# Optimization experiments

Hardware: AMD Instinct MI355X
Metric: run time of the kernel (lower is better)

Reference implementation:

```python
import jax, jax.numpy as jnp
import numpy as np

N_NODE = 4096   # nodes per graph (generalized from hardcoded 55)
IN_DIM = 200    # input_dim, forced by attn1 in_channel=200
OUT_DIM = 200   # output_dim, forced equal to input_dim by GRU_gate shapes
N_HEADS = 8     # forced by attn2 in_channel 1600 = 8*200
SEQ_LEN = 4
HID = 200       # hid_units default


def _glorot(k, shape):
    r = np.sqrt(6.0 / (shape[0] + shape[1])).astype(np.float32)
    return jax.random.uniform(k, shape, jnp.float32, -r, r)


def setup_inputs() -> dict:
    key = jax.random.key(0)
    ks = jax.random.split(key, 32)
    inp = {}
    mask = jax.random.bernoulli(ks[0], 0.01, (SEQ_LEN, N_NODE, N_NODE))
    inp['adjs'] = jax.random.uniform(ks[1], (SEQ_LEN, N_NODE, N_NODE), jnp.float32) * mask
    inp['feats'] = jax.random.normal(ks[2], (SEQ_LEN, N_NODE, IN_DIM), jnp.float32)
    inp['p_covss'] = jnp.zeros((SEQ_LEN,), jnp.float32)  # passed but unused in original
    # per-head weight_vars, randn(output_dim, input_dim) in original call()
    inp['init_wv'] = jax.random.normal(ks[3], (N_HEADS, OUT_DIM, IN_DIM), jnp.float32)
    # attn1 (shared across all heads): conv1d(k=1) == linear
    inp['W1'] = _glorot(ks[4], (HID, IN_DIM)); inp['b1'] = jnp.zeros((HID,), jnp.float32)
    inp['a11'] = _glorot(ks[5], (HID, 1))[:, 0]; inp['a11b'] = jnp.zeros((), jnp.float32)
    inp['a12'] = _glorot(ks[6], (HID, 1))[:, 0]; inp['a12b'] = jnp.zeros((), jnp.float32)
    # attn2
    inp['W2'] = _glorot(ks[7], (OUT_DIM, N_HEADS * HID)); inp['b2'] = jnp.zeros((OUT_DIM,), jnp.float32)
    inp['a21'] = _glorot(ks[8], (OUT_DIM, 1))[:, 0]; inp['a21b'] = jnp.zeros((), jnp.float32)
    inp['a22'] = _glorot(ks[9], (OUT_DIM, 1))[:, 0]; inp['a22b'] = jnp.zeros((), jnp.float32)
    # GRU gates (reset/update/htilda), reduce=True since n_node != input_dim
    for i, g in enumerate(['r', 'u', 'h']):
        inp['W' + g] = _glorot(ks[10 + 4 * i], (N_NODE, OUT_DIM))
        inp['U' + g] = _glorot(ks[11 + 4 * i], (OUT_DIM, OUT_DIM))
        inp['P' + g] = _glorot(ks[12 + 4 * i], (IN_DIM, N_NODE))
        inp['b' + g] = jnp.zeros((IN_DIM, OUT_DIM), jnp.float32)
    return inp


def reference(adjs, feats, p_covss, init_wv, W1, b1, a11, a11b, a12, a12b,
              W2, b2, a21, a21b, a22, a22b,
              Wr, Ur, Pr, br, Wu, Uu, Pu, bu, Wh, Uh, Ph, bh):
    def gat(x):  # x: [N, IN_DIM]
        fts = x @ W1.T + b1                                   # [N, HID]
        # logits f_1 + f_2^T on [N,1,1] stays [N,1,1]; softmax over the
        # singleton dim is identically 1 -> attention is degenerate.
        s = jax.nn.leaky_relu((fts @ a11 + a11b) + (fts @ a12 + a12b), 0.01)
        coefs = jnp.ones_like(s)                              # softmax([N,1,1], dim=1)
        h = jax.nn.elu(coefs[:, None] * fts)                  # [N, HID]
        hcat = jnp.tile(h, (1, N_HEADS))                      # heads share attn1 -> identical
        fts2 = hcat @ W2.T + b2                               # [N, OUT_DIM]
        s2 = jax.nn.leaky_relu((fts2 @ a21 + a21b) + (fts2 @ a22 + a22b), 0.01)
        coefs2 = jnp.ones_like(s2)
        out = jax.nn.elu(coefs2[:, None] * fts2)              # [N, OUT_DIM]
        # torch: out.view(nb_classes, -1).T then softmax(dim=1), then view(-1, out_dim)
        logits = jnp.reshape(out, (OUT_DIM, N_NODE)).T        # memory reinterpretation, not transpose
        return jax.nn.softmax(logits, axis=1)                 # [N, OUT_DIM]

    embeds = jax.vmap(gat)(feats)                             # [T, N, OUT_DIM]

    def gru_step(wv, adj):  # wv: [H, OUT_DIM, IN_DIM=OUT_DIM], adj: [N, N]
        # head-independent sparse propagation bases, one per gate
        gr = Pr @ (adj @ Wr) + br                             # [IN_DIM, OUT_DIM]
        gu = Pu @ (adj @ Wu) + bu
        gh = Ph @ (adj @ Wh) + bh
        r = jax.nn.sigmoid(gr + wv @ Ur)                      # [H, 200, 200]
        u = jax.nn.sigmoid(gu + wv @ Uu)
        hcap = jnp.tanh(gh + (r * wv) @ Uh)
        return (1.0 - u) * wv + u * hcap, None

    final_wv, _ = jax.lax.scan(gru_step, init_wv, adjs[1:])   # evolve over t=1..T-1
    return embeds, final_wv
```

## Files before the change

### kernel.cpp

```cpp
#include <hip/hip_runtime.h>
#include <hip/hip_bf16.h>
#include <math.h>

typedef __hip_bfloat16 bf16;
typedef __attribute__((ext_vector_type(8))) short short8;
typedef __attribute__((ext_vector_type(4))) float f32x4;

#define N_NODE 4096
#define DIM 200
#define NH 8
#define SEQ 4
#define TLDA 40

__device__ __forceinline__ float eluf(float x) { return x > 0.f ? x : expm1f(x); }
__device__ __forceinline__ float sigm(float x) { return 1.f / (1.f + expf(-x)); }

template<bool ISB>
__device__ __forceinline__ float ldv(const void* p, size_t i) {
    if (ISB) return __bfloat162float(((const bf16*)p)[i]);
    else     return ((const float*)p)[i];
}
template<bool ISB>
__device__ __forceinline__ void stv(void* p, size_t i, float v) {
    if (ISB) ((bf16*)p)[i] = __float2bfloat16(v);
    else     ((float*)p)[i] = v;
}
__device__ __forceinline__ float bflo(unsigned u) { return __uint_as_float((u & 0xffffu) << 16); }
__device__ __forceinline__ float bfhi(unsigned u) { return __uint_as_float(u & 0xffff0000u); }
__device__ __forceinline__ short f2bs(float v) {
    bf16 h = __float2bfloat16(v);
    return *(short*)&h;
}

__global__ void k_detect(const void* feats, int* flag) {
    __shared__ int cnt;
    if (threadIdx.x == 0) cnt = 0;
    __syncthreads();
    const unsigned short* u = (const unsigned short*)feats;
    unsigned short v = u[2 * threadIdx.x];
    int e = (v >> 7) & 0xFF;
    if (e >= 100 && e <= 140) atomicAdd(&cnt, 1);
    __syncthreads();
    if (threadIdx.x == 0) *flag = (cnt >= 128) ? 1 : 0;
}


template<int AMODE>
__device__ __forceinline__ short8 ldA8x(const void* A, int lda, int arow, bool rowOK,
                                        int kk, int K) {
    short8 r;
    if (rowOK && kk + 8 <= K) {
        if (AMODE == 1) {
            r = *(const short8*)((const short*)A + (size_t)arow * lda + kk);
        } else {
            const float* ap = (const float*)A + (size_t)arow * lda + kk;
            float4 f0 = *(const float4*)ap;
            float4 f1 = *(const float4*)(ap + 4);
            r[0] = f2bs(f0.x); r[1] = f2bs(f0.y); r[2] = f2bs(f0.z); r[3] = f2bs(f0.w);
            r[4] = f2bs(f1.x); r[5] = f2bs(f1.y); r[6] = f2bs(f1.z); r[7] = f2bs(f1.w);
        }
    } else {
#pragma unroll
        for (int j = 0; j < 8; j++) {
            bool ok = rowOK && kk + j < K;
            if (AMODE == 1) r[j] = ok ? ((const short*)A)[(size_t)arow * lda + kk + j] : (short)0;
            else            r[j] = ok ? f2bs(((const float*)A)[(size_t)arow * lda + kk + j]) : (short)0;
        }
    }
    return r;
}

template<int BMODE>
__device__ __forceinline__ short8 ldB8x(const void* B, int gcol, bool colOK,
                                        int kk, int K) {
    short8 r;
    if (BMODE == 2) {
        if (colOK && kk + 8 <= K) {
            r = *(const short8*)((const short*)B + (size_t)gcol * K + kk);
        } else {
#pragma unroll
            for (int j = 0; j < 8; j++)
                r[j] = (colOK && kk + j < K) ? ((const short*)B)[(size_t)gcol * K + kk + j] : (short)0;
        }
    } else {
#pragma unroll
        for (int j = 0; j < 8; j++)
            r[j] = (colOK && kk + j < K) ? ((const short*)B)[(size_t)(kk + j) * DIM + gcol] : (short)0;
    }
    return r;
}

__device__ __forceinline__ short8 ldUfrag(const short* U, int col, int k) {
    if (k + 8 <= 200) return *(const short8*)(U + col * 200 + k);
    short8 z = {};
    return z;
}

template<int EPI, int AMODE, int BMODE, int CB16>
__device__ void mgemm(short* As, short* Bs,
                      const void* A, int lda, const void* B, int M, int K,
                      int kbeg, int kend, const float* X1,
                      void* Cv, int row0, int c0) {
    const int N = DIM;
    int tid = threadIdx.x;
    int wave = tid >> 6, lane = tid & 63;
    int m16 = lane & 15, q = lane >> 4;
    int s_row = tid >> 2;
    int s_k   = (tid & 3) * 8;
    int b_col = tid & 63;
    int b_kg  = (tid >> 6) * 8;
    int arow = row0 + s_row;
    bool rowOK = arow < M;
    int gcol = c0 + b_col;
    bool colOK = gcol < N;
    short8 la = ldA8x<AMODE>(A, lda, arow, rowOK, kbeg + s_k, K);
    short8 lb = ldB8x<BMODE>(B, gcol, colOK, kbeg + b_kg, K);
    f32x4 acc[4] = {};
    for (int k0 = kbeg; k0 < kend; k0 += 32) {
        __syncthreads();
        *(short8*)&As[s_row * TLDA + s_k] = la;
        *(short8*)&Bs[b_col * TLDA + b_kg] = lb;
        __syncthreads();
        int kn = k0 + 32;
        if (kn < kend) {
            la = ldA8x<AMODE>(A, lda, arow, rowOK, kn + s_k, K);
            lb = ldB8x<BMODE>(B, gcol, colOK, kn + b_kg, K);
        }
        short8 bfr = *(short8*)&Bs[(wave * 16 + m16) * TLDA + q * 8];
#pragma unroll
        for (int r = 0; r < 4; r++) {
            short8 af = *(short8*)&As[(r * 16 + m16) * TLDA + q * 8];
            acc[r] = __builtin_amdgcn_mfma_f32_16x16x32_bf16(af, bfr, acc[r], 0, 0, 0);
        }
    }
    int colw = c0 + wave * 16 + m16;
    if (colw >= N) return;
#pragma unroll
    for (int r = 0; r < 4; r++) {
        int rowb = row0 + r * 16 + q * 4;
#pragma unroll
        for (int reg = 0; reg < 4; reg++) {
            int row = rowb + reg;
            if (row >= M) continue;
            float v = acc[r][reg];
            size_t ci = (size_t)row * 200 + colw;
            if (EPI == 0) {
                float o = eluf(v + X1[colw]);
                if (CB16) ((short*)Cv)[ci] = f2bs(o);
                else      ((float*)Cv)[ci] = o;
            } else {
                atomicAdd(&((float*)Cv)[ci], v);
            }
        }
    }
}

template<bool ISB>
__device__ void aw_body(char* smemc, const void* adjs, const unsigned short* Wcat,
                        bf16* AWb, int i, int s) {
    size_t arow = ((size_t)(s + 1) * N_NODE + i) * N_NODE;
    int*   s_k   = (int*)smemc;
    float* s_v   = (float*)(smemc + 2048);
    int*   s_cnt = (int*)(smemc + 4096);
    int tid = threadIdx.x;
    if (tid == 0) *s_cnt = 0;
    __syncthreads();
    float vals[16];
#pragma unroll
    for (int c = 0; c < 4; c++) {
        int col = c * 1024 + tid * 4;
        if (ISB) {
            ushort4 u = *(const ushort4*)((const unsigned short*)adjs + arow + col);
            vals[c*4+0] = __uint_as_float((unsigned)u.x << 16);
            vals[c*4+1] = __uint_as_float((unsigned)u.y << 16);
            vals[c*4+2] = __uint_as_float((unsigned)u.z << 16);
            vals[c*4+3] = __uint_as_float((unsigned)u.w << 16);
        } else {
            float4 f = *(const float4*)((const float*)adjs + arow + col);
            vals[c*4+0] = f.x; vals[c*4+1] = f.y; vals[c*4+2] = f.z; vals[c*4+3] = f.w;
        }
    }
#pragma unroll
    for (int q = 0; q < 16; q++) {
        if (vals[q] != 0.f) {
            int p = atomicAdd(s_cnt, 1);
            if (p < 512) { s_k[p] = (q >> 2) * 1024 + tid * 4 + (q & 3); s_v[p] = vals[q]; }
        }
    }
    __syncthreads();
    int n = *s_cnt < 512 ? *s_cnt : 512;
    float a0 = 0.f, a1 = 0.f, d0 = 0.f, d1 = 0.f;
    bool hasB = (tid < 44);
    int offA = 2 * tid, offB = 512 + 2 * tid;
    int e = 0;
    for (; e + 4 <= n; e += 4) {
        int   k0 = s_k[e],   k1 = s_k[e+1], k2 = s_k[e+2], k3 = s_k[e+3];
        float v0 = s_v[e],   v1 = s_v[e+1], v2 = s_v[e+2], v3 = s_v[e+3];
        unsigned wa0 = *(const unsigned*)(Wcat + (size_t)k0 * 608 + offA);
        unsigned wa1 = *(const unsigned*)(Wcat + (size_t)k1 * 608 + offA);
        unsigned wa2 = *(const unsigned*)(Wcat + (size_t)k2 * 608 + offA);
        unsigned wa3 = *(const unsigned*)(Wcat + (size_t)k3 * 608 + offA);
        if (hasB) {
            unsigned wb0 = *(const unsigned*)(Wcat + (size_t)k0 * 608 + offB);
            unsigned wb1 = *(const unsigned*)(Wcat + (size_t)k1 * 608 + offB);
            unsigned wb2 = *(const unsigned*)(Wcat + (size_t)k2 * 608 + offB);
            unsigned wb3 = *(const unsigned*)(Wcat + (size_t)k3 * 608 + offB);
            d0 += v0*bflo(wb0) + v1*bflo(wb1) + v2*bflo(wb2) + v3*bflo(wb3);
            d1 += v0*bfhi(wb0) + v1*bfhi(wb1) + v2*bfhi(wb2) + v3*bfhi(wb3);
        }
        a0 += v0*bflo(wa0) + v1*bflo(wa1) + v2*bflo(wa2) + v3*bflo(wa3);
        a1 += v0*bfhi(wa0) + v1*bfhi(wa1) + v2*bfhi(wa2) + v3*bfhi(wa3);
    }
    for (; e < n; e++) {
        int k = s_k[e]; float v = s_v[e];
        unsigned wa = *(const unsigned*)(Wcat + (size_t)k * 608 + offA);
        a0 += v * bflo(wa); a1 += v * bfhi(wa);
        if (hasB) {
            unsigned wb = *(const unsigned*)(Wcat + (size_t)k * 608 + offB);
            d0 += v * bflo(wb); d1 += v * bfhi(wb);
        }
    }
    int gA = (offA < 200) ? 0 : (offA < 400 ? 1 : 2);
    int oA = offA - gA * 200;
    size_t wbase = ((size_t)(s * 3 + gA) * N_NODE + i) * DIM + oA;
    AWb[wbase]     = __float2bfloat16(a0);
    AWb[wbase + 1] = __float2bfloat16(a1);
    if (hasB) {
        int oB = offB - 400;
        size_t wb2 = ((size_t)(s * 3 + 2) * N_NODE + i) * DIM + oB;
        AWb[wb2]     = __float2bfloat16(d0);
        AWb[wb2 + 1] = __float2bfloat16(d1);
    }
}

template<bool ISB>
__device__ void softmax_body(char* smemc, const float* O, void* out, int t, int i0) {
    float* tile   = (float*)smemc;
    float* pm     = tile + 13000;
    float* ps     = pm + 256;
    float* sm_m   = ps + 256;
    float* sm_inv = sm_m + 64;
    const float* ob = O + (size_t)t * N_NODE * DIM;
    int tid = threadIdx.x;
    for (int idx = tid; idx < 200 * 64; idx += 256) {
        int j = idx >> 6, c = idx & 63;
        tile[j * 65 + c] = ob[(size_t)j * N_NODE + i0 + c];
    }
    __syncthreads();
    int g = tid >> 6, lane = tid & 63;
    int j0 = g * 50, j1 = j0 + 50;
    float mp = -1e30f;
    for (int j = j0; j < j1; j++) mp = fmaxf(mp, tile[j * 65 + lane]);
    pm[g * 64 + lane] = mp;
    __syncthreads();
    if (tid < 64)
        sm_m[tid] = fmaxf(fmaxf(pm[tid], pm[64 + tid]), fmaxf(pm[128 + tid], pm[192 + tid]));
    __syncthreads();
    float mv = sm_m[lane];
    float sp = 0.f;
    for (int j = j0; j < j1; j++) {
        float e = expf(tile[j * 65 + lane] - mv);
        tile[j * 65 + lane] = e;
        sp += e;
    }
    ps[g * 64 + lane] = sp;
    __syncthreads();
    if (tid < 64)
        sm_inv[tid] = 1.f / (ps[tid] + ps[64 + tid] + ps[128 + tid] + ps[192 + tid]);
    __syncthreads();
    size_t ob2 = ((size_t)t * N_NODE + i0) * DIM;
    for (int idx = tid; idx < 64 * 200; idx += 256) {
        int il = idx / 200, j = idx - il * 200;
        stv<ISB>(out, ob2 + (size_t)il * DIM + j, tile[j * 65 + il] * sm_inv[il]);
    }
}

__global__ __launch_bounds__(256) void k_L2(const int* fl, const void* feats,
        const short* W1b, const float* b1f, short* Hb,
        const void* adjs, const unsigned short* Wcat, bf16* AWb) {
    __shared__ __align__(16) char smem[10752];
    int b = blockIdx.x;
    if (b < 1024) {
        short* As = (short*)smem;
        short* Bs = As + 64 * TLDA;
        int row0 = (b >> 2) * 64, c0 = (b & 3) * 64;
        if (*fl)
            mgemm<0, 1, 2, 1>(As, Bs, feats, DIM, W1b, SEQ * N_NODE, DIM, 0, DIM,
                              b1f, Hb, row0, c0);
        else
            mgemm<0, 0, 2, 1>(As, Bs, feats, DIM, W1b, SEQ * N_NODE, DIM, 0, DIM,
                              b1f, Hb, row0, c0);
    } else {
        int ab = b - 1024;
        int i = ab & 4095, s = ab >> 12;
        if (*fl) aw_body<true >(smem, adjs, Wcat, AWb, i, s);
        else     aw_body<false>(smem, adjs, Wcat, AWb, i, s);
    }
}

__global__ __launch_bounds__(256) void k_L3(const int* fl, const short* Hb,
        const short* W2b, const float* b2f, float* Obuf,
        const void* P0, const void* P1, const void* P2, const bf16* AWb, float* G) {
    __shared__ __align__(16) char smem[10752];
    short* As = (short*)smem;
    short* Bs = As + 64 * TLDA;
    int b = blockIdx.x;
    if (b < 1024) {
        int row0 = (b >> 2) * 64, c0 = (b & 3) * 64;
        mgemm<0, 1, 2, 0>(As, Bs, Hb, DIM, W2b, SEQ * N_NODE, DIM, 0, DIM,
                          b2f, Obuf, row0, c0);
    } else {
        int pb = b - 1024;
        int z = pb >> 4, rest = pb & 15;
        int row0 = (rest >> 2) * 64, c0 = (rest & 3) * 64;
        int sg = z >> 3, split = z & 7;
        int g = sg - (sg / 3) * 3;
        const void* A = (g == 0) ? P0 : (g == 1) ? P1 : P2;
        const void* B = AWb + (size_t)sg * N_NODE * DIM;
        float* C = G + (size_t)sg * DIM * DIM;
        int kbeg = split * (N_NODE / 8), kend = kbeg + N_NODE / 8;
        if (*fl) mgemm<4, 1, 1, 0>(As, Bs, A, N_NODE, B, DIM, N_NODE, kbeg, kend,
                                   nullptr, C, row0, c0);
        else     mgemm<4, 0, 1, 0>(As, Bs, A, N_NODE, B, DIM, N_NODE, kbeg, kend,
                                   nullptr, C, row0, c0);
    }
}

#define GRU_NB 50
#define WSTR 232
__global__ __launch_bounds__(256) void k_gru(const int* fl, const float* Obuf,
        void* out_, const short* Ub, const float* G,
        const float* wv_g, const short* wvb_g) {
    __shared__ __align__(16) char smem[80896];
    int b = blockIdx.x;
    if (b >= GRU_NB) {
        int sb = b - GRU_NB;
        int t = sb >> 6, i0 = (sb & 63) * 64;
        if (*fl) softmax_body<true >(smem, Obuf, out_, t, i0);
        else     softmax_body<false>(smem, Obuf, out_, t, i0);
        return;
    }
    float* wvf  = (float*)smem;
    float* ulds = (float*)(smem + 25600);
    short* wvbl = (short*)(smem + 51200);
    short* rwbl = (short*)(smem + 66048);
    int tid = threadIdx.x;
    int grow0 = b * 32;
    for (int idx = tid; idx < 32 * 200; idx += 256) {
        int row = idx / 200, col = idx - row * 200;
        wvf[idx] = wv_g[(size_t)(grow0 + row) * 200 + col];
        wvbl[row * WSTR + col] = wvb_g[(size_t)(grow0 + row) * 200 + col];
    }
    for (int idx = tid; idx < 32 * 32; idx += 256) {
        int row = idx >> 5, j = idx & 31;
        wvbl[row * WSTR + 200 + j] = 0;
        rwbl[row * WSTR + 200 + j] = 0;
    }
    int wave = tid >> 6, lane = tid & 63;
    int m16 = lane & 15, q = lane >> 4;
    const short* Urb = Ub;
    const short* Uub = Ub + 40000;
    const short* Uhb = Ub + 80000;
    int fdt = *fl;
    __syncthreads();
    for (int s = 0; s < 3; s++) {
        const float* Gr = G + (size_t)(s * 3 + 0) * 40000;
        const float* Gu = G + (size_t)(s * 3 + 1) * 40000;
        const float* Gh = G + (size_t)(s * 3 + 2) * 40000;
#pragma unroll
        for (int ct = 0; ct < 4; ct++) {
            int colw = ct * 64 + wave * 16 + m16;
            short8 brf[7], buf_[7];
#pragma unroll
            for (int kc = 0; kc < 7; kc++) {
                brf[kc]  = ldUfrag(Urb, colw, kc * 32 + q * 8);
                buf_[kc] = ldUfrag(Uub, colw, kc * 32 + q * 8);
            }
            f32x4 accR[2] = {}, accU[2] = {};
#pragma unroll
            for (int kc = 0; kc < 7; kc++) {
#pragma unroll
                for (int r = 0; r < 2; r++) {
                    short8 af = *(short8*)&wvbl[(r * 16 + m16) * WSTR + kc * 32 + q * 8];
                    accR[r] = __builtin_amdgcn_mfma_f32_16x16x32_bf16(af, brf[kc],  accR[r], 0, 0, 0);
                    accU[r] = __builtin_amdgcn_mfma_f32_16x16x32_bf16(af, buf_[kc], accU[r], 0, 0, 0);
                }
            }
            if (colw < 200) {
#pragma unroll
                for (int r = 0; r < 2; r++) {
#pragma unroll
                    for (int reg = 0; reg < 4; reg++) {
                        int row = r * 16 + q * 4 + reg;
                        int a200 = (grow0 + row) % 200;
                        float rw = sigm(Gr[a200 * 200 + colw] + accR[r][reg]) * wvf[row * 200 + colw];
                        rwbl[row * WSTR + colw] = f2bs(rw);
                        ulds[row * 200 + colw] = sigm(Gu[a200 * 200 + colw] + accU[r][reg]);
                    }
                }
            }
        }
        __syncthreads();
#pragma unroll
        for (int ct = 0; ct < 4; ct++) {
            int colw = ct * 64 + wave * 16 + m16;
            short8 bhf[7];
#pragma unroll
            for (int kc = 0; kc < 7; kc++)
                bhf[kc] = ldUfrag(Uhb, colw, kc * 32 + q * 8);
            f32x4 acc[2] = {};
#pragma unroll
            for (int kc = 0; kc < 7; kc++) {
#pragma unroll
                for (int r = 0; r < 2; r++) {
                    short8 af = *(short8*)&rwbl[(r * 16 + m16) * WSTR + kc * 32 + q * 8];
                    acc[r] = __builtin_amdgcn_mfma_f32_16x16x32_bf16(af, bhf[kc], acc[r], 0, 0, 0);
                }
            }
            if (colw < 200) {
#pragma unroll
                for (int r = 0; r < 2; r++) {
#pragma unroll
                    for (int reg = 0; reg < 4; reg++) {
                        int row = r * 16 + q * 4 + reg;
                        int grow = grow0 + row;
                        int a200 = grow % 200;
                        float uu = ulds[row * 200 + colw];
                        float hc = tanhf(Gh[a200 * 200 + colw] + acc[r][reg]);
                        float nv = (1.f - uu) * wvf[row * 200 + colw] + uu * hc;
                        wvf[row * 200 + colw] = nv;
                        wvbl[row * WSTR + colw] = f2bs(nv);
                        if (s == 2) {
                            size_t oo = (size_t)SEQ * N_NODE * DIM + (size_t)grow * 200 + colw;
                            if (fdt) stv<true>(out_, oo, nv); else stv<false>(out_, oo, nv);
                        }
                    }
                }
            }
        }
        __syncthreads();
    }
}

template<bool ISB>
__device__ void prep_body(const void* W1, const void* b1, const void* W2, const void* b2,
                          const void* Ur, const void* Uu, const void* Uh,
                          const void* br, const void* bu, const void* bh,
                          const void* iwv, const void* Wr, const void* Wu, const void* Wh,
                          short* W1b, short* W2b, float* b1f, float* b2f,
                          short* Ub, float* wv, short* wvb, float* G, unsigned short* Wcat) {
    int idx = blockIdx.x * 256 + threadIdx.x;
    if (idx < 40000) {
        W1b[idx] = f2bs(ldv<ISB>(W1, idx));
    } else if (idx < 80000) {
        int r = idx - 40000;
        int n = r / 200, k = r - n * 200;
        float s = 0.f;
        for (int h = 0; h < NH; h++) s += ldv<ISB>(W2, (size_t)n * 1600 + h * 200 + k);
        W2b[r] = f2bs(s);
    } else if (idx < 80512) {
        int j = idx - 80000;
        if (j < 256)      b1f[j] = (j < 200) ? ldv<ISB>(b1, j) : 0.f;
        else              b2f[j - 256] = (j - 256 < 200) ? ldv<ISB>(b2, j - 256) : 0.f;
    } else if (idx < 200512) {
        int j = idx - 80512;
        int g = j / 40000, r = j - g * 40000;
        int n = r / 200, k = r - n * 200;
        const void* U = (g == 0) ? Ur : (g == 1) ? Uu : Uh;
        Ub[j] = f2bs(ldv<ISB>(U, (size_t)k * 200 + n));
    } else if (idx < 520512) {
        int j = idx - 200512;
        float v = ldv<ISB>(iwv, j);
        wv[j] = v;
        wvb[j] = f2bs(v);
    } else if (idx < 880512) {
        int j = idx - 520512;
        int sg = j / 40000, r = j - sg * 40000;
        int g = sg - (sg / 3) * 3;
        const void* bb = (g == 0) ? br : (g == 1) ? bu : bh;
        G[j] = ldv<ISB>(bb, r);
    } else {
        int j = idx - 880512;
        if (j < 4096 * 600) {
            int k = j / 600, c = j - k * 600;
            int g = (c < 200) ? 0 : (c < 400 ? 1 : 2);
            int o = c - g * 200;
            const void* W = (g == 0) ? Wr : (g == 1) ? Wu : Wh;
            bf16 v = __float2bfloat16(ldv<ISB>(W, (size_t)k * 200 + o));
            Wcat[(size_t)k * 608 + c] = *(unsigned short*)&v;
        }
    }
}
__global__ void k_prep(const int* fl, const void* W1, const void* b1, const void* W2,
                       const void* b2, const void* Ur, const void* Uu, const void* Uh,
                       const void* br, const void* bu, const void* bh, const void* iwv,
                       const void* Wr, const void* Wu, const void* Wh,
                       short* W1b, short* W2b, float* b1f, float* b2f,
                       short* Ub, float* wv, short* wvb, float* G, unsigned short* Wcat) {
    if (*fl) prep_body<true >(W1, b1, W2, b2, Ur, Uu, Uh, br, bu, bh, iwv, Wr, Wu, Wh,
                              W1b, W2b, b1f, b2f, Ub, wv, wvb, G, Wcat);
    else     prep_body<false>(W1, b1, W2, b2, Ur, Uu, Uh, br, bu, bh, iwv, Wr, Wu, Wh,
                              W1b, W2b, b1f, b2f, Ub, wv, wvb, G, Wcat);
}

extern "C" void kernel_launch(void* const* d_in, const int* in_sizes, int n_in,
                              void* d_out, int out_size, void* d_ws, size_t ws_size,
                              hipStream_t stream) {
    const void* adjs    = d_in[0];
    const void* feats   = d_in[1];
    const void* init_wv = d_in[3];
    const void* W1 = d_in[4];
    const void* b1 = d_in[5];
    const void* W2 = d_in[10];
    const void* b2 = d_in[11];
    const void* Wr = d_in[16];
    const void* Ur = d_in[17];
    const void* Pr = d_in[18];
    const void* br = d_in[19];
    const void* Wu = d_in[20];
    const void* Uu = d_in[21];
    const void* Pu = d_in[22];
    const void* bu = d_in[23];
    const void* Wh = d_in[24];
    const void* Uh = d_in[25];
    const void* Ph = d_in[26];
    const void* bh = d_in[27];

    int*   flag = (int*)d_ws;
    float* base = (float*)d_ws;
    unsigned short* Wcat = (unsigned short*)(base + 64);
    bf16*  AWb  = (bf16*)(base + 1245248);
    short* Hb   = (short*)(base + 4931648);
    float* Obuf = base + 6570048;
    short* W1b  = (short*)(base + 9846848);
    short* W2b  = (short*)(base + 9866848);
    float* b1f  = base + 9886848;
    float* b2f  = base + 9887104;
    short* Ub   = (short*)(base + 9887360);
    float* G    = base + 9947360;
    float* wv   = base + 10307360;
    short* wvb  = (short*)(base + 10627360);

    k_detect<<<1, 256, 0, stream>>>(feats, flag);
    k_prep<<<(3338112 + 255) / 256, 256, 0, stream>>>(
        flag, W1, b1, W2, b2, Ur, Uu, Uh, br, bu, bh, init_wv, Wr, Wu, Wh,
        W1b, W2b, b1f, b2f, Ub, wv, wvb, G, Wcat);

    k_L2<<<1024 + 3 * N_NODE, 256, 0, stream>>>(flag, feats, W1b, b1f, Hb, adjs, Wcat, AWb);

    k_L3<<<1024 + 1152, 256, 0, stream>>>(flag, Hb, W2b, b2f, Obuf, Pr, Pu, Ph, AWb, G);

    k_gru<<<GRU_NB + 256, 256, 0, stream>>>(flag, Obuf, d_out, Ub, G, wv, wvb);
}
```

Baseline: 628.4 us.

## Fuse GAT two-layer MLP per row tile and split GRU into multi-block kernels

The two GAT linear layers are fused into one block body that keeps the hidden tile in shared memory, so the intermediate Hb no longer round-trips through global memory and the second layer no longer waits for a separate kernel. The GRU, which previously ran on only 50 blocks looping three steps, is split into per-step e12/e3 kernels over a 4x25 grid, with the reset-gated product and the update gate staged in global buffers. The propagation GEMM moves to its own 3D-grid kernel. This raises parallelism in the GRU phase but adds more kernel launches and global traffic for the intermediates.

```diff
diff --git a/kernel.cpp b/kernel.cpp
--- a/kernel.cpp
+++ b/kernel.cpp
@@ -44,6 +44,12 @@
     if (threadIdx.x == 0) *flag = (cnt >= 128) ? 1 : 0;
 }
 
+
+__device__ __forceinline__ short8 ldfrag200(const short* P, int row, int k) {
+    if (k + 8 <= 200) return *(const short8*)(P + (size_t)row * 200 + k);
+    short8 z = {};
+    return z;
+}
 
 template<int AMODE>
 __device__ __forceinline__ short8 ldA8x(const void* A, int lda, int arow, bool rowOK,
@@ -70,38 +76,19 @@
     return r;
 }
 
-template<int BMODE>
-__device__ __forceinline__ short8 ldB8x(const void* B, int gcol, bool colOK,
+__device__ __forceinline__ short8 ldB8s(const short* B, int gcol, bool colOK,
                                         int kk, int K) {
     short8 r;
-    if (BMODE == 2) {
-        if (colOK && kk + 8 <= K) {
-            r = *(const short8*)((const short*)B + (size_t)gcol * K + kk);
-        } else {
-#pragma unroll
-            for (int j = 0; j < 8; j++)
-                r[j] = (colOK && kk + j < K) ? ((const short*)B)[(size_t)gcol * K + kk + j] : (short)0;
-        }
-    } else {
-#pragma unroll
-        for (int j = 0; j < 8; j++)
-            r[j] = (colOK && kk + j < K) ? ((const short*)B)[(size_t)(kk + j) * DIM + gcol] : (short)0;
-    }
+#pragma unroll
+    for (int j = 0; j < 8; j++)
+        r[j] = (colOK && kk + j < K) ? B[(size_t)(kk + j) * DIM + gcol] : (short)0;
     return r;
 }
 
-__device__ __forceinline__ short8 ldUfrag(const short* U, int col, int k) {
-    if (k + 8 <= 200) return *(const short8*)(U + col * 200 + k);
-    short8 z = {};
-    return z;
-}
-
-template<int EPI, int AMODE, int BMODE, int CB16>
-__device__ void mgemm(short* As, short* Bs,
-                      const void* A, int lda, const void* B, int M, int K,
-                      int kbeg, int kend, const float* X1,
-                      void* Cv, int row0, int c0) {
-    const int N = DIM;
+template<int AMODE>
+__device__ void pg_gemm(short* As, short* Bs, const void* A, const short* B,
+                        int kbeg, int kend, float* C, int row0, int c0) {
+    const int M = DIM, K = N_NODE;
     int tid = threadIdx.x;
     int wave = tid >> 6, lane = tid & 63;
     int m16 = lane & 15, q = lane >> 4;
@@ -112,9 +99,9 @@
     int arow = row0 + s_row;
     bool rowOK = arow < M;
     int gcol = c0 + b_col;
-    bool colOK = gcol < N;
-    short8 la = ldA8x<AMODE>(A, lda, arow, rowOK, kbeg + s_k, K);
-    short8 lb = ldB8x<BMODE>(B, gcol, colOK, kbeg + b_kg, K);
+    bool colOK = gcol < DIM;
+    short8 la = ldA8x<AMODE>(A, K, arow, rowOK, kbeg + s_k, K);
+    short8 lb = ldB8s(B, gcol, colOK, kbeg + b_kg, K);
     f32x4 acc[4] = {};
     for (int k0 = kbeg; k0 < kend; k0 += 32) {
         __syncthreads();
@@ -123,8 +110,8 @@
         __syncthreads();
         int kn = k0 + 32;
         if (kn < kend) {
-            la = ldA8x<AMODE>(A, lda, arow, rowOK, kn + s_k, K);
-            lb = ldB8x<BMODE>(B, gcol, colOK, kn + b_kg, K);
+            la = ldA8x<AMODE>(A, K, arow, rowOK, kn + s_k, K);
+            lb = ldB8s(B, gcol, colOK, kn + b_kg, K);
         }
         short8 bfr = *(short8*)&Bs[(wave * 16 + m16) * TLDA + q * 8];
 #pragma unroll
@@ -134,7 +121,7 @@
         }
     }
     int colw = c0 + wave * 16 + m16;
-    if (colw >= N) return;
+    if (colw >= DIM) return;
 #pragma unroll
     for (int r = 0; r < 4; r++) {
         int rowb = row0 + r * 16 + q * 4;
@@ -142,15 +129,7 @@
         for (int reg = 0; reg < 4; reg++) {
             int row = rowb + reg;
             if (row >= M) continue;
-            float v = acc[r][reg];
-            size_t ci = (size_t)row * 200 + colw;
-            if (EPI == 0) {
-                float o = eluf(v + X1[colw]);
-                if (CB16) ((short*)Cv)[ci] = f2bs(o);
-                else      ((float*)Cv)[ci] = o;
-            } else {
-                atomicAdd(&((float*)Cv)[ci], v);
-            }
+            atomicAdd(&C[(size_t)row * 200 + colw], acc[r][reg]);
         }
     }
 }
@@ -234,6 +213,89 @@
 }
 
 template<bool ISB>
+__device__ void gat_body(char* smemc, const void* feats, const short* W1b, const float* b1f,
+                         const short* W2b, const float* b2f, float* Obuf, int row0) {
+    short* Af = (short*)smemc;
+    short* Hs = (short*)(smemc + 14848);
+    int tid = threadIdx.x;
+    for (int idx = tid; idx < 32 * 32; idx += 256) {
+        int row = idx >> 5, j = idx & 31;
+        Af[row * 232 + 200 + j] = 0;
+        Hs[row * 232 + 200 + j] = 0;
+    }
+    for (int g = tid; g < 800; g += 256) {
+        int row = g / 25, kg = (g - row * 25) * 8;
+        if (ISB) {
+            *(short8*)&Af[row * 232 + kg] =
+                *(const short8*)((const short*)feats + (size_t)(row0 + row) * 200 + kg);
+        } else {
+            const float* fp = (const float*)feats + (size_t)(row0 + row) * 200 + kg;
+            float4 f0 = *(const float4*)fp, f1 = *(const float4*)(fp + 4);
+            short8 r;
+            r[0] = f2bs(f0.x); r[1] = f2bs(f0.y); r[2] = f2bs(f0.z); r[3] = f2bs(f0.w);
+            r[4] = f2bs(f1.x); r[5] = f2bs(f1.y); r[6] = f2bs(f1.z); r[7] = f2bs(f1.w);
+            *(short8*)&Af[row * 232 + kg] = r;
+        }
+    }
+    __syncthreads();
+    int wave = tid >> 6, lane = tid & 63;
+    int m16 = lane & 15, q = lane >> 4;
+#pragma unroll
+    for (int ct = 0; ct < 4; ct++) {
+        int colw = ct * 64 + wave * 16 + m16;
+        short8 bf1[7];
+#pragma unroll
+        for (int kc = 0; kc < 7; kc++) bf1[kc] = ldfrag200(W1b, colw, kc * 32 + q * 8);
+        f32x4 acc[2] = {};
+#pragma unroll
+        for (int kc = 0; kc < 7; kc++) {
+#pragma unroll
+            for (int r = 0; r < 2; r++) {
+                short8 af = *(short8*)&Af[(r * 16 + m16) * 232 + kc * 32 + q * 8];
+                acc[r] = __builtin_amdgcn_mfma_f32_16x16x32_bf16(af, bf1[kc], acc[r], 0, 0, 0);
+            }
+        }
+        if (colw < 200) {
+#pragma unroll
+            for (int r = 0; r < 2; r++) {
+#pragma unroll
+                for (int reg = 0; reg < 4; reg++) {
+                    int row = r * 16 + q * 4 + reg;
+                    Hs[row * 232 + colw] = f2bs(eluf(acc[r][reg] + b1f[colw]));
+                }
+            }
+        }
+    }
+    __syncthreads();
+#pragma unroll
+    for (int ct = 0; ct < 4; ct++) {
+        int colw = ct * 64 + wave * 16 + m16;
+        short8 bf2[7];
+#pragma unroll
+        for (int kc = 0; kc < 7; kc++) bf2[kc] = ldfrag200(W2b, colw, kc * 32 + q * 8);
+        f32x4 acc[2] = {};
+#pragma unroll
+        for (int kc = 0; kc < 7; kc++) {
+#pragma unroll
+            for (int r = 0; r < 2; r++) {
+                short8 af = *(short8*)&Hs[(r * 16 + m16) * 232 + kc * 32 + q * 8];
+                acc[r] = __builtin_amdgcn_mfma_f32_16x16x32_bf16(af, bf2[kc], acc[r], 0, 0, 0);
+            }
+        }
+        if (colw < 200) {
+#pragma unroll
+            for (int r = 0; r < 2; r++) {
+#pragma unroll
+                for (int reg = 0; reg < 4; reg++) {
+                    int row = r * 16 + q * 4 + reg;
+                    Obuf[(size_t)(row0 + row) * 200 + colw] = eluf(acc[r][reg] + b2f[colw]);
+                }
+            }
+        }
+    }
+}
+
+template<bool ISB>
 __device__ void softmax_body(char* smemc, const float* O, void* out, int t, int i0) {
     float* tile   = (float*)smemc;
     float* pm     = tile + 13000;
@@ -275,171 +337,148 @@
     }
 }
 
-__global__ __launch_bounds__(256) void k_L2(const int* fl, const void* feats,
-        const short* W1b, const float* b1f, short* Hb,
-        const void* adjs, const unsigned short* Wcat, bf16* AWb) {
-    __shared__ __align__(16) char smem[10752];
+__device__ __forceinline__ void e12_core(const short* wvb, const short* Urb, const short* Uub,
+        const float* Gr, const float* Gu, const float* wvf, short* rwb, float* u,
+        int row0, int c0) {
+    int tid = threadIdx.x;
+    int wave = tid >> 6, lane = tid & 63;
+    int m16 = lane & 15, q = lane >> 4;
+    int colw = c0 + wave * 16 + m16;
+    short8 br_[7], bu_[7];
+#pragma unroll
+    for (int kc = 0; kc < 7; kc++) {
+        br_[kc] = ldfrag200(Urb, colw, kc * 32 + q * 8);
+        bu_[kc] = ldfrag200(Uub, colw, kc * 32 + q * 8);
+    }
+    f32x4 accR[4] = {}, accU[4] = {};
+#pragma unroll
+    for (int kc = 0; kc < 7; kc++) {
+#pragma unroll
+        for (int r = 0; r < 4; r++) {
+            short8 af = ldfrag200(wvb, row0 + r * 16 + m16, kc * 32 + q * 8);
+            accR[r] = __builtin_amdgcn_mfma_f32_16x16x32_bf16(af, br_[kc], accR[r], 0, 0, 0);
+            accU[r] = __builtin_amdgcn_mfma_f32_16x16x32_bf16(af, bu_[kc], accU[r], 0, 0, 0);
+        }
+    }
+    if (colw >= 200) return;
+#pragma unroll
+    for (int r = 0; r < 4; r++) {
+#pragma unroll
+        for (int reg = 0; reg < 4; reg++) {
+            int row = row0 + r * 16 + q * 4 + reg;
+            int a200 = row - (row / 200) * 200;
+            size_t ci = (size_t)row * 200 + colw;
+            rwb[ci] = f2bs(sigm(Gr[a200 * 200 + colw] + accR[r][reg]) * wvf[ci]);
+            u[ci]   = sigm(Gu[a200 * 200 + colw] + accU[r][reg]);
+        }
+    }
+}
+
+template<bool ISB>
+__device__ __forceinline__ void e3_core(const short* rwb, const short* Uhb,
+        const float* Gh, const float* ubuf, float* wv, void* out2, short* wvb,
+        int row0, int c0) {
+    int tid = threadIdx.x;
+    int wave = tid >> 6, lane = tid & 63;
+    int m16 = lane & 15, q = lane >> 4;
+    int colw = c0 + wave * 16 + m16;
+    short8 bh_[7];
+#pragma unroll
+    for (int kc = 0; kc < 7; kc++)
+        bh_[kc] = ldfrag200(Uhb, colw, kc * 32 + q * 8);
+    f32x4 acc[4] = {};
+#pragma unroll
+    for (int kc = 0; kc < 7; kc++) {
+#pragma unroll
+        for (int r = 0; r < 4; r++) {
+            short8 af = ldfrag200(rwb, row0 + r * 16 + m16, kc * 32 + q * 8);
+            acc[r] = __builtin_amdgcn_mfma_f32_16x16x32_bf16(af, bh_[kc], acc[r], 0, 0, 0);
+        }
+    }
+    if (colw >= 200) return;
+#pragma unroll
+    for (int r = 0; r < 4; r++) {
+#pragma unroll
+        for (int reg = 0; reg < 4; reg++) {
+            int row = row0 + r * 16 + q * 4 + reg;
+            int a200 = row - (row / 200) * 200;
+            size_t ci = (size_t)row * 200 + colw;
+            float uu = ubuf[ci];
+            float hc = tanhf(Gh[a200 * 200 + colw] + acc[r][reg]);
+            float nv = (1.f - uu) * wv[ci] + uu * hc;
+            wv[ci] = nv;
+            wvb[ci] = f2bs(nv);
+            if (out2) {
+                size_t oo = (size_t)SEQ * N_NODE * DIM + ci;
+                stv<ISB>(out2, oo, nv);
+            }
+        }
+    }
+}
+
+__global__ __launch_bounds__(256) void k_A(const int* fl, const void* feats,
+        const short* W1b, const float* b1f, const short* W2b, const float* b2f,
+        float* Obuf, const void* adjs, const unsigned short* Wcat, bf16* AWb) {
+    __shared__ __align__(16) char smem[29696];
     int b = blockIdx.x;
-    if (b < 1024) {
-        short* As = (short*)smem;
-        short* Bs = As + 64 * TLDA;
-        int row0 = (b >> 2) * 64, c0 = (b & 3) * 64;
-        if (*fl)
-            mgemm<0, 1, 2, 1>(As, Bs, feats, DIM, W1b, SEQ * N_NODE, DIM, 0, DIM,
-                              b1f, Hb, row0, c0);
-        else
-            mgemm<0, 0, 2, 1>(As, Bs, feats, DIM, W1b, SEQ * N_NODE, DIM, 0, DIM,
-                              b1f, Hb, row0, c0);
+    if (b < 512) {
+        if (*fl) gat_body<true >(smem, feats, W1b, b1f, W2b, b2f, Obuf, b * 32);
+        else     gat_body<false>(smem, feats, W1b, b1f, W2b, b2f, Obuf, b * 32);
     } else {
-        int ab = b - 1024;
+        int ab = b - 512;
         int i = ab & 4095, s = ab >> 12;
         if (*fl) aw_body<true >(smem, adjs, Wcat, AWb, i, s);
         else     aw_body<false>(smem, adjs, Wcat, AWb, i, s);
     }
 }
 
-__global__ __launch_bounds__(256) void k_L3(const int* fl, const short* Hb,
-        const short* W2b, const float* b2f, float* Obuf,
-        const void* P0, const void* P1, const void* P2, const bf16* AWb, float* G) {
+__global__ __launch_bounds__(256) void k_pg(const int* fl,
+        const void* P0, const void* P1, const void* P2,
+        const bf16* AWb, float* G) {
     __shared__ __align__(16) char smem[10752];
     short* As = (short*)smem;
     short* Bs = As + 64 * TLDA;
+    int z = blockIdx.z;
+    int sg = z >> 3, split = z & 7;
+    int g = sg - (sg / 3) * 3;
+    const void* A = (g == 0) ? P0 : (g == 1) ? P1 : P2;
+    const short* B = (const short*)(AWb + (size_t)sg * N_NODE * DIM);
+    float* C = G + (size_t)sg * DIM * DIM;
+    int row0 = blockIdx.y * 64, c0 = blockIdx.x * 64;
+    int kbeg = split * (N_NODE / 8), kend = kbeg + N_NODE / 8;
+    if (*fl) pg_gemm<1>(As, Bs, A, B, kbeg, kend, C, row0, c0);
+    else     pg_gemm<0>(As, Bs, A, B, kbeg, kend, C, row0, c0);
+}
+
+__global__ __launch_bounds__(256) void k_e12sm(const int* fl, const float* Obuf,
+        void* out_, const short* wvb, const short* Ub, const float* G,
+        const float* wv, short* rwb, float* ubuf) {
     int b = blockIdx.x;
-    if (b < 1024) {
-        int row0 = (b >> 2) * 64, c0 = (b & 3) * 64;
-        mgemm<0, 1, 2, 0>(As, Bs, Hb, DIM, W2b, SEQ * N_NODE, DIM, 0, DIM,
-                          b2f, Obuf, row0, c0);
+    if (b < 100) {
+        e12_core(wvb, Ub, Ub + 40000, G, G + 40000, wv, rwb, ubuf,
+                 (b >> 2) * 64, (b & 3) * 64);
     } else {
-        int pb = b - 1024;
-        int z = pb >> 4, rest = pb & 15;
-        int row0 = (rest >> 2) * 64, c0 = (rest & 3) * 64;
-        int sg = z >> 3, split = z & 7;
-        int g = sg - (sg / 3) * 3;
-        const void* A = (g == 0) ? P0 : (g == 1) ? P1 : P2;
-        const void* B = AWb + (size_t)sg * N_NODE * DIM;
-        float* C = G + (size_t)sg * DIM * DIM;
-        int kbeg = split * (N_NODE / 8), kend = kbeg + N_NODE / 8;
-        if (*fl) mgemm<4, 1, 1, 0>(As, Bs, A, N_NODE, B, DIM, N_NODE, kbeg, kend,
-                                   nullptr, C, row0, c0);
-        else     mgemm<4, 0, 1, 0>(As, Bs, A, N_NODE, B, DIM, N_NODE, kbeg, kend,
-                                   nullptr, C, row0, c0);
-    }
-}
-
-#define GRU_NB 50
-#define WSTR 232
-__global__ __launch_bounds__(256) void k_gru(const int* fl, const float* Obuf,
-        void* out_, const short* Ub, const float* G,
-        const float* wv_g, const short* wvb_g) {
-    __shared__ __align__(16) char smem[80896];
-    int b = blockIdx.x;
-    if (b >= GRU_NB) {
-        int sb = b - GRU_NB;
+        __shared__ __align__(16) char smem[54784];
+        int sb = b - 100;
         int t = sb >> 6, i0 = (sb & 63) * 64;
         if (*fl) softmax_body<true >(smem, Obuf, out_, t, i0);
         else     softmax_body<false>(smem, Obuf, out_, t, i0);
-        return;
-    }
-    float* wvf  = (float*)smem;
-    float* ulds = (float*)(smem + 25600);
-    short* wvbl = (short*)(smem + 51200);
-    short* rwbl = (short*)(smem + 66048);
-    int tid = threadIdx.x;
-    int grow0 = b * 32;
-    for (int idx = tid; idx < 32 * 200; idx += 256) {
-        int row = idx / 200, col = idx - row * 200;
-        wvf[idx] = wv_g[(size_t)(grow0 + row) * 200 + col];
-        wvbl[row * WSTR + col] = wvb_g[(size_t)(grow0 + row) * 200 + col];
-    }
-    for (int idx = tid; idx < 32 * 32; idx += 256) {
-        int row = idx >> 5, j = idx & 31;
-        wvbl[row * WSTR + 200 + j] = 0;
-        rwbl[row * WSTR + 200 + j] = 0;
-    }
-    int wave = tid >> 6, lane = tid & 63;
-    int m16 = lane & 15, q = lane >> 4;
-    const short* Urb = Ub;
-    const short* Uub = Ub + 40000;
-    const short* Uhb = Ub + 80000;
-    int fdt = *fl;
-    __syncthreads();
-    for (int s = 0; s < 3; s++) {
-        const float* Gr = G + (size_t)(s * 3 + 0) * 40000;
-        const float* Gu = G + (size_t)(s * 3 + 1) * 40000;
-        const float* Gh = G + (size_t)(s * 3 + 2) * 40000;
-#pragma unroll
-        for (int ct = 0; ct < 4; ct++) {
-            int colw = ct * 64 + wave * 16 + m16;
-            short8 brf[7], buf_[7];
-#pragma unroll
-            for (int kc = 0; kc < 7; kc++) {
-                brf[kc]  = ldUfrag(Urb, colw, kc * 32 + q * 8);
-                buf_[kc] = ldUfrag(Uub, colw, kc * 32 + q * 8);
-            }
-            f32x4 accR[2] = {}, accU[2] = {};
-#pragma unroll
-            for (int kc = 0; kc < 7; kc++) {
-#pragma unroll
-                for (int r = 0; r < 2; r++) {
-                    short8 af = *(short8*)&wvbl[(r * 16 + m16) * WSTR + kc * 32 + q * 8];
-                    accR[r] = __builtin_amdgcn_mfma_f32_16x16x32_bf16(af, brf[kc],  accR[r], 0, 0, 0);
-                    accU[r] = __builtin_amdgcn_mfma_f32_16x16x32_bf16(af, buf_[kc], accU[r], 0, 0, 0);
-                }
-            }
-            if (colw < 200) {
-#pragma unroll
-                for (int r = 0; r < 2; r++) {
-#pragma unroll
-                    for (int reg = 0; reg < 4; reg++) {
-                        int row = r * 16 + q * 4 + reg;
-                        int a200 = (grow0 + row) % 200;
-                        float rw = sigm(Gr[a200 * 200 + colw] + accR[r][reg]) * wvf[row * 200 + colw];
-                        rwbl[row * WSTR + colw] = f2bs(rw);
-                        ulds[row * 200 + colw] = sigm(Gu[a200 * 200 + colw] + accU[r][reg]);
-                    }
-                }
-            }
-        }
-        __syncthreads();
-#pragma unroll
-        for (int ct = 0; ct < 4; ct++) {
-            int colw = ct * 64 + wave * 16 + m16;
-            short8 bhf[7];
-#pragma unroll
-            for (int kc = 0; kc < 7; kc++)
-                bhf[kc] = ldUfrag(Uhb, colw, kc * 32 + q * 8);
-            f32x4 acc[2] = {};
-#pragma unroll
-            for (int kc = 0; kc < 7; kc++) {
-#pragma unroll
-                for (int r = 0; r < 2; r++) {
-                    short8 af = *(short8*)&rwbl[(r * 16 + m16) * WSTR + kc * 32 + q * 8];
-                    acc[r] = __builtin_amdgcn_mfma_f32_16x16x32_bf16(af, bhf[kc], acc[r], 0, 0, 0);
-                }
-            }
-            if (colw < 200) {
-#pragma unroll
-                for (int r = 0; r < 2; r++) {
-#pragma unroll
-                    for (int reg = 0; reg < 4; reg++) {
-                        int row = r * 16 + q * 4 + reg;
-                        int grow = grow0 + row;
-                        int a200 = grow % 200;
-                        float uu = ulds[row * 200 + colw];
-                        float hc = tanhf(Gh[a200 * 200 + colw] + acc[r][reg]);
-                        float nv = (1.f - uu) * wvf[row * 200 + colw] + uu * hc;
-                        wvf[row * 200 + colw] = nv;
-                        wvbl[row * WSTR + colw] = f2bs(nv);
-                        if (s == 2) {
-                            size_t oo = (size_t)SEQ * N_NODE * DIM + (size_t)grow * 200 + colw;
-                            if (fdt) stv<true>(out_, oo, nv); else stv<false>(out_, oo, nv);
-                        }
-                    }
-                }
-            }
-        }
-        __syncthreads();
-    }
+    }
+}
+
+__global__ __launch_bounds__(256) void k_e12(const short* wvb, const short* Ub,
+        const float* Gr, const float* Gu, const float* wv, short* rwb, float* ubuf) {
+    e12_core(wvb, Ub, Ub + 40000, Gr, Gu, wv, rwb, ubuf,
+             blockIdx.y * 64, blockIdx.x * 64);
+}
+
+__global__ __launch_bounds__(256) void k_e3(const short* rwb, const short* Uhb,
+        const float* Gh, const float* ubuf, float* wv, const int* fl, void* out2,
+        short* wvb) {
+    int row0 = blockIdx.y * 64, c0 = blockIdx.x * 64;
+    if (out2 && *fl) e3_core<true >(rwb, Uhb, Gh, ubuf, wv, out2, wvb, row0, c0);
+    else if (out2)   e3_core<false>(rwb, Uhb, Gh, ubuf, wv, out2, wvb, row0, c0);
+    else             e3_core<false>(rwb, Uhb, Gh, ubuf, wv, nullptr, wvb, row0, c0);
 }
 
 template<bool ISB>
@@ -530,7 +569,6 @@
     float* base = (float*)d_ws;
     unsigned short* Wcat = (unsigned short*)(base + 64);
     bf16*  AWb  = (bf16*)(base + 1245248);
-    short* Hb   = (short*)(base + 4931648);
     float* Obuf = base + 6570048;
     short* W1b  = (short*)(base + 9846848);
     short* W2b  = (short*)(base + 9866848);
@@ -540,15 +578,34 @@
     float* G    = base + 9947360;
     float* wv   = base + 10307360;
     short* wvb  = (short*)(base + 10627360);
+    float* ubuf = base + 10787360;
+    short* rwb  = (short*)(base + 11107360);
 
     k_detect<<<1, 256, 0, stream>>>(feats, flag);
     k_prep<<<(3338112 + 255) / 256, 256, 0, stream>>>(
         flag, W1, b1, W2, b2, Ur, Uu, Uh, br, bu, bh, init_wv, Wr, Wu, Wh,
         W1b, W2b, b1f, b2f, Ub, wv, wvb, G, Wcat);
 
-    k_L2<<<1024 + 3 * N_NODE, 256, 0, stream>>>(flag, feats, W1b, b1f, Hb, adjs, Wcat, AWb);
-
-    k_L3<<<1024 + 1152, 256, 0, stream>>>(flag, Hb, W2b, b2f, Obuf, Pr, Pu, Ph, AWb, G);
-
-    k_gru<<<GRU_NB + 256, 256, 0, stream>>>(flag, Obuf, d_out, Ub, G, wv, wvb);
-}
+    k_A<<<512 + 3 * N_NODE, 256, 0, stream>>>(flag, feats, W1b, b1f, W2b, b2f,
+                                              Obuf, adjs, Wcat, AWb);
+
+    {
+        dim3 g(4, 4, 72);
+        k_pg<<<g, 256, 0, stream>>>(flag, Pr, Pu, Ph, AWb, G);
+    }
+
+    k_e12sm<<<356, 256, 0, stream>>>(flag, Obuf, d_out, wvb, Ub, G, wv, rwb, ubuf);
+    {
+        dim3 g(4, 25);
+        for (int s = 0; s < 3; s++) {
+            const float* Gh = G + (size_t)(s * 3 + 2) * DIM * DIM;
+            void* out2 = (s == 2) ? d_out : nullptr;
+            k_e3<<<g, 256, 0, stream>>>(rwb, Ub + 80000, Gh, ubuf, wv, flag, out2, wvb);
+            if (s < 2) {
+                const float* Gr = G + (size_t)((s + 1) * 3 + 0) * DIM * DIM;
+                const float* Gu = G + (size_t)((s + 1) * 3 + 1) * DIM * DIM;
+                k_e12<<<g, 256, 0, stream>>>(wvb, Ub, Gr, Gu, wv, rwb, ubuf);
+            }
+        }
+    }
+}
```

After: 605.4 us. 1.04x faster.
